# Performance work log

Measured on AMD Instinct MI355X. Metric: run time of the kernel, lower is better.

Reference implementation:

```python
import jax, jax.numpy as jnp
import numpy as np

N = 100_000   # nodes
E = 3_200_000 # edges (avg degree 32)
IN, HID, OUT = 1433, 16, 7  # hardcoded in Method_GCN_Class.__init__


def setup_inputs() -> dict:
    key = jax.random.key(0)
    ks = jax.random.split(key, 6)
    x = jax.random.normal(ks[0], (N, IN), dtype=jnp.float32)
    adj_row = jax.random.randint(ks[1], (E,), 0, N, dtype=jnp.int32)
    adj_col = jax.random.randint(ks[2], (E,), 0, N, dtype=jnp.int32)
    adj_val = jax.random.uniform(ks[3], (E,), dtype=jnp.float32)
    W1 = jax.random.uniform(ks[4], (IN, HID), dtype=jnp.float32)  # nn.init.uniform_
    b1 = jnp.zeros((HID,), dtype=jnp.float32)
    W2 = jax.random.uniform(ks[5], (HID, OUT), dtype=jnp.float32)
    b2 = jnp.zeros((OUT,), dtype=jnp.float32)
    return dict(x=x, adj_row=adj_row, adj_col=adj_col, adj_val=adj_val,
                W1=W1, b1=b1, W2=W2, b2=b2)


def _spmm(row, col, val, dense):
    # torch.sparse.mm(adj, dense) with adj in COO form: out[r] += val*dense[c]
    return jax.ops.segment_sum(val[:, None] * dense[col], row, num_segments=N)


def reference(x, adj_row, adj_col, adj_val, W1, b1, W2, b2):
    # layer 1: graph_conv -> relu (dropout p=0.1 is a no-op at inference)
    h = _spmm(adj_row, adj_col, adj_val, x @ W1) + b1
    h = jax.nn.relu(h)
    # layer 2: graph_conv -> log_softmax over classes
    h = _spmm(adj_row, adj_col, adj_val, h @ W2) + b2
    return jax.nn.log_softmax(h, axis=1)
```

## Files before the change

kernel.cpp:

```cpp
#include <hip/hip_runtime.h>
#include <math.h>

#define IN_F 1433
#define HID  16
#define OUTC 7
#define SCAN_T 1024

#define K1_THREADS 512
#define K1_ROWS_W  8
#define K1_ROWS_B  64
#define KA         768
#define LDSW       17
#define K1_LDS_FLOATS (KA * LDSW)

#define SLOT_C   44
#define OVF_CAP  131072

typedef float f4_t __attribute__((ext_vector_type(4)));
typedef f4_t uf4 __attribute__((aligned(4)));

__host__ __device__ __forceinline__ int imin(int a, int b) { return a < b ? a : b; }

__global__ __launch_bounds__(256) void zero_i32(int4* __restrict__ p, int n4)
{
    int i = blockIdx.x * blockDim.x + threadIdx.x;
    if (i < n4) p[i] = make_int4(0, 0, 0, 0);
}

__device__ __forceinline__ void k1_body(
    const float* __restrict__ x, const float* __restrict__ W1,
    float* __restrict__ XW, int N, int vbid, float* sW)
{
    const int wave = threadIdx.x >> 6;
    const int lane = threadIdx.x & 63;
    const int ks   = lane & 15;
    const int j4   = lane >> 4;
    const int row0 = vbid * K1_ROWS_B + wave * K1_ROWS_W;

    int xoff[K1_ROWS_W];
#pragma unroll
    for (int r = 0; r < K1_ROWS_W; ++r) {
        int row = row0 + r;
        if (row > N - 1) row = N - 1;
        if (row < 0) row = 0;
        xoff[r] = row * IN_F;
    }

    float acc[K1_ROWS_W][4];
#pragma unroll
    for (int r = 0; r < K1_ROWS_W; ++r)
#pragma unroll
        for (int jj = 0; jj < 4; ++jj) acc[r][jj] = 0.f;

#pragma unroll 1
    for (int p = 0; p < 2; ++p) {
        const int pbase = p ? KA : 0;
        const int pk    = p ? (IN_F - KA) : KA;
        if (p) __syncthreads();
        for (int f = threadIdx.x; f < pk * HID; f += K1_THREADS)
            sW[(f >> 4) * LDSW + (f & 15)] = W1[pbase * HID + f];
        __syncthreads();

        const int nfull = pk >> 6;
#pragma unroll 1
        for (int c = 0; c < nfull; ++c) {
            const int kb = c * 64 + ks * 4;
            uf4 xq[K1_ROWS_W];
#pragma unroll
            for (int r = 0; r < K1_ROWS_W; ++r)
                xq[r] = *(const uf4*)(x + (size_t)xoff[r] + pbase + kb);
            float w[4][4];
#pragma unroll
            for (int kk = 0; kk < 4; ++kk) {
                const float* wr = sW + (size_t)(kb + kk) * LDSW + j4 * 4;
                w[kk][0] = wr[0]; w[kk][1] = wr[1];
                w[kk][2] = wr[2]; w[kk][3] = wr[3];
            }
#pragma unroll
            for (int kk = 0; kk < 4; ++kk)
#pragma unroll
                for (int r = 0; r < K1_ROWS_W; ++r) {
                    const float xv = xq[r][kk];
                    acc[r][0] += xv * w[kk][0];
                    acc[r][1] += xv * w[kk][1];
                    acc[r][2] += xv * w[kk][2];
                    acc[r][3] += xv * w[kk][3];
                }
        }

        const int tb = nfull * 64 + ks * 4;
        if (tb < pk + 3 && (pk & 63)) {
#pragma unroll
            for (int kk = 0; kk < 4; ++kk) {
                const int kloc = tb + kk;
                const bool ok = (kloc < pk);
                const float* wr = sW + (size_t)kloc * LDSW + j4 * 4;
                float w0 = wr[0], w1 = wr[1], w2 = wr[2], w3 = wr[3];
#pragma unroll
                for (int r = 0; r < K1_ROWS_W; ++r) {
                    const float xv = ok ? x[(size_t)xoff[r] + pbase + kloc] : 0.f;
                    acc[r][0] += xv * w0;
                    acc[r][1] += xv * w1;
                    acc[r][2] += xv * w2;
                    acc[r][3] += xv * w3;
                }
            }
        }
    }

#pragma unroll
    for (int m = 1; m <= 8; m <<= 1)
#pragma unroll
        for (int r = 0; r < K1_ROWS_W; ++r)
#pragma unroll
            for (int jj = 0; jj < 4; ++jj)
                acc[r][jj] += __shfl_xor(acc[r][jj], m);

    if (ks == 0) {
#pragma unroll
        for (int r = 0; r < K1_ROWS_W; ++r) {
            const int row = row0 + r;
            if (row >= 0 && row < N) {
                float4 o = make_float4(acc[r][0], acc[r][1], acc[r][2], acc[r][3]);
                *(float4*)(XW + (size_t)row * HID + j4 * 4) = o;
            }
        }
    }
}

__device__ __forceinline__ void scatter_slots_body(
    const int* __restrict__ arow, const int* __restrict__ acol,
    const float* __restrict__ aval, int* __restrict__ cnt,
    int2* __restrict__ slots, int* __restrict__ ovf, int* __restrict__ ovfc,
    int E, int sb, int nsb)
{
    const int tid = sb * K1_THREADS + threadIdx.x;
    const int stride = nsb * K1_THREADS;
    const int E4 = E >> 2;
    const int4*   ar4 = (const int4*)arow;
    const int4*   ac4 = (const int4*)acol;
    const float4* av4 = (const float4*)aval;
    for (int v = tid; v < E4; v += stride) {
        int4 r = ar4[v];
        int4 c = ac4[v];
        float4 val = av4[v];
        int rr[4] = {r.x, r.y, r.z, r.w};
        int cc[4] = {c.x, c.y, c.z, c.w};
        float vv[4] = {val.x, val.y, val.z, val.w};
#pragma unroll
        for (int u = 0; u < 4; ++u) {
            int pos = atomicAdd(&cnt[rr[u]], 1);
            if (pos < SLOT_C) {
                slots[(size_t)rr[u] * SLOT_C + pos] =
                    make_int2(cc[u], __float_as_int(vv[u]));
            } else {
                int op = atomicAdd(ovfc, 1);
                if (op < OVF_CAP) {
                    ovf[3 * op]     = rr[u];
                    ovf[3 * op + 1] = cc[u];
                    ovf[3 * op + 2] = __float_as_int(vv[u]);
                }
            }
        }
    }
    for (int v = E4 * 4 + tid; v < E; v += stride) {
        int rr = arow[v];
        int pos = atomicAdd(&cnt[rr], 1);
        if (pos < SLOT_C) {
            slots[(size_t)rr * SLOT_C + pos] =
                make_int2(acol[v], __float_as_int(aval[v]));
        } else {
            int op = atomicAdd(ovfc, 1);
            if (op < OVF_CAP) {
                ovf[3 * op]     = rr;
                ovf[3 * op + 1] = acol[v];
                ovf[3 * op + 2] = __float_as_int(aval[v]);
            }
        }
    }
}

__global__ __launch_bounds__(K1_THREADS) void k1_scatter_slots(
    const float* __restrict__ x, const float* __restrict__ W1,
    float* __restrict__ XW, int N, int k1b,
    const int* __restrict__ arow, const int* __restrict__ acol,
    const float* __restrict__ aval, int* __restrict__ cnt,
    int2* __restrict__ slots, int* __restrict__ ovf, int* __restrict__ ovfc,
    int E, int scb)
{
    __shared__ float sW[K1_LDS_FLOATS];
    const int bid = blockIdx.x;
    if ((bid % 3 == 2) && (bid / 3 < scb)) {
        scatter_slots_body(arow, acol, aval, cnt, slots, ovf, ovfc, E, bid / 3, scb);
        return;
    }
    const int k1_idx = bid - imin((bid + 1) / 3, scb);
    if (k1_idx >= k1b) return;
    k1_body(x, W1, XW, N, k1_idx, sW);
}

__global__ __launch_bounds__(256) void ovf_apply16(
    const int* __restrict__ ovf, const int* __restrict__ ovfc,
    const float* __restrict__ XW, float* __restrict__ Hx)
{
    const int n = imin(ovfc[0], OVF_CAP);
    const int tid = blockIdx.x * blockDim.x + threadIdx.x;
    const int stride = gridDim.x * blockDim.x;
    for (int i = tid; i < n; i += stride) {
        const int r = ovf[3 * i], c = ovf[3 * i + 1];
        const float v = __int_as_float(ovf[3 * i + 2]);
        const float* src = XW + (size_t)c * HID;
        float* dst = Hx + (size_t)r * HID;
#pragma unroll
        for (int j = 0; j < HID; ++j) atomicAdd(dst + j, v * src[j]);
    }
}

__global__ __launch_bounds__(256) void ovf_apply7(
    const int* __restrict__ ovf, const int* __restrict__ ovfc,
    const float* __restrict__ h2, float* __restrict__ Ox)
{
    const int n = imin(ovfc[0], OVF_CAP);
    const int tid = blockIdx.x * blockDim.x + threadIdx.x;
    const int stride = gridDim.x * blockDim.x;
    for (int i = tid; i < n; i += stride) {
        const int r = ovf[3 * i], c = ovf[3 * i + 1];
        const float v = __int_as_float(ovf[3 * i + 2]);
        const float* src = h2 + (size_t)c * 8;
        float* dst = Ox + (size_t)r * 8;
#pragma unroll
        for (int j = 0; j < OUTC; ++j) atomicAdd(dst + j, v * src[j]);
    }
}

__global__ __launch_bounds__(256) void spmm16_slots(
    const int* __restrict__ cnt, const int2* __restrict__ slots,
    const float* __restrict__ XW, const float* __restrict__ Hx,
    const float* __restrict__ b1, const float* __restrict__ W2,
    float* __restrict__ h2, int N)
{
    const int gw = (int)((blockIdx.x * (size_t)blockDim.x + threadIdx.x) >> 6);
    if (gw >= N) return;
    const int lane = threadIdx.x & 63;
    const int j = lane & 15;
    const int w = lane >> 4;
    int deg = cnt[gw]; deg = deg < SLOT_C ? deg : SLOT_C;
    const int2* base = slots + (size_t)gw * SLOT_C;

    float acc = 0.f;
    int k = w * 4;
    while (k + 4 <= deg) {
        const int4* q = (const int4*)(base + k);
        int4 A = q[0], B = q[1];
        acc += __int_as_float(A.y) * XW[(size_t)A.x * HID + j];
        acc += __int_as_float(A.w) * XW[(size_t)A.z * HID + j];
        acc += __int_as_float(B.y) * XW[(size_t)B.x * HID + j];
        acc += __int_as_float(B.w) * XW[(size_t)B.z * HID + j];
        k += 16;
    }
    for (; k < deg; ++k) {
        int2 a = base[k];
        acc += __int_as_float(a.y) * XW[(size_t)a.x * HID + j];
    }
    acc += __shfl_xor(acc, 16);
    acc += __shfl_xor(acc, 32);
    acc += Hx[(size_t)gw * HID + j];

    const float h = fmaxf(acc + b1[j], 0.f);
    float p[OUTC];
#pragma unroll
    for (int c = 0; c < OUTC; ++c) p[c] = h * W2[j * OUTC + c];
#pragma unroll
    for (int m = 1; m <= 8; m <<= 1)
#pragma unroll
        for (int c = 0; c < OUTC; ++c) p[c] += __shfl_xor(p[c], m);

    if (lane < 8) {
        float o = p[0];
        o = (lane == 1) ? p[1] : o;
        o = (lane == 2) ? p[2] : o;
        o = (lane == 3) ? p[3] : o;
        o = (lane == 4) ? p[4] : o;
        o = (lane == 5) ? p[5] : o;
        o = (lane == 6) ? p[6] : o;
        if (lane == 7) o = 0.f;
        h2[(size_t)gw * 8 + lane] = o;
    }
}

__global__ __launch_bounds__(256) void spmm7_slots(
    const int* __restrict__ cnt, const int2* __restrict__ slots,
    const float* __restrict__ h2, const float* __restrict__ Ox,
    const float* __restrict__ b2, float* __restrict__ out, int N)
{
    const int gw = (int)((blockIdx.x * (size_t)blockDim.x + threadIdx.x) >> 6);
    if (gw >= N) return;
    const int lane = threadIdx.x & 63;
    const int j = lane & 7;
    const int w = lane >> 3;
    int deg = cnt[gw]; deg = deg < SLOT_C ? deg : SLOT_C;
    const int2* base = slots + (size_t)gw * SLOT_C;

    float acc = 0.f;
    int k = w * 4;
    while (k + 4 <= deg) {
        const int4* q = (const int4*)(base + k);
        int4 A = q[0], B = q[1];
        acc += __int_as_float(A.y) * h2[(size_t)A.x * 8 + j];
        acc += __int_as_float(A.w) * h2[(size_t)A.z * 8 + j];
        acc += __int_as_float(B.y) * h2[(size_t)B.x * 8 + j];
        acc += __int_as_float(B.w) * h2[(size_t)B.z * 8 + j];
        k += 32;
    }
    for (; k < deg; ++k) {
        int2 a = base[k];
        acc += __int_as_float(a.y) * h2[(size_t)a.x * 8 + j];
    }
    acc += __shfl_xor(acc, 8);
    acc += __shfl_xor(acc, 16);
    acc += __shfl_xor(acc, 32);
    acc += Ox[(size_t)gw * 8 + j];

    const float bias = b2[(j < OUTC) ? j : 0];
    const float val  = acc + bias;
    float mx = (j < OUTC) ? val : -INFINITY;
    mx = fmaxf(mx, __shfl_xor(mx, 1));
    mx = fmaxf(mx, __shfl_xor(mx, 2));
    mx = fmaxf(mx, __shfl_xor(mx, 4));
    float ex = (j < OUTC) ? expf(val - mx) : 0.f;
    ex += __shfl_xor(ex, 1);
    ex += __shfl_xor(ex, 2);
    ex += __shfl_xor(ex, 4);
    if (lane < OUTC) out[(size_t)gw * OUTC + lane] = val - mx - logf(ex);
}

__device__ __forceinline__ void hist_body(
    const int* __restrict__ arow, int* __restrict__ cnt, int E, int hb, int nhb)
{
    const int tid = hb * K1_THREADS + threadIdx.x;
    const int stride = nhb * K1_THREADS;
    const int E4 = E >> 2;
    const int4* a4 = (const int4*)arow;
    for (int v = tid; v < E4; v += stride) {
        int4 r = a4[v];
        atomicAdd(&cnt[r.x], 1);
        atomicAdd(&cnt[r.y], 1);
        atomicAdd(&cnt[r.z], 1);
        atomicAdd(&cnt[r.w], 1);
    }
    for (int v = E4 * 4 + tid; v < E; v += stride) atomicAdd(&cnt[arow[v]], 1);
}

__device__ __forceinline__ void scatter_body(
    const int* __restrict__ arow, const int* __restrict__ acol,
    const float* __restrict__ aval, int* __restrict__ cursor,
    int2* __restrict__ ecv, int E, int sb, int nsb)
{
    const int tid = sb * K1_THREADS + threadIdx.x;
    const int stride = nsb * K1_THREADS;
    const int E4 = E >> 2;
    const int4*   ar4 = (const int4*)arow;
    const int4*   ac4 = (const int4*)acol;
    const float4* av4 = (const float4*)aval;
    for (int v = tid; v < E4; v += stride) {
        int4 r = ar4[v];
        int4 c = ac4[v];
        float4 val = av4[v];
        int p0 = atomicAdd(&cursor[r.x], 1);
        int p1 = atomicAdd(&cursor[r.y], 1);
        int p2 = atomicAdd(&cursor[r.z], 1);
        int p3 = atomicAdd(&cursor[r.w], 1);
        ecv[p0] = make_int2(c.x, __float_as_int(val.x));
        ecv[p1] = make_int2(c.y, __float_as_int(val.y));
        ecv[p2] = make_int2(c.z, __float_as_int(val.z));
        ecv[p3] = make_int2(c.w, __float_as_int(val.w));
    }
    for (int v = E4 * 4 + tid; v < E; v += stride) {
        int pos = atomicAdd(&cursor[arow[v]], 1);
        ecv[pos] = make_int2(acol[v], __float_as_int(aval[v]));
    }
}

__global__ __launch_bounds__(K1_THREADS) void k1_hist_fused(
    const float* __restrict__ x, const float* __restrict__ W1,
    float* __restrict__ XW, int N, int half1,
    const int* __restrict__ arow, int* __restrict__ cnt, int E, int histB)
{
    __shared__ float sW[K1_LDS_FLOATS];
    const int bid = blockIdx.x;
    if ((bid % 3 == 2) && (bid / 3 < histB)) {
        hist_body(arow, cnt, E, bid / 3, histB);
        return;
    }
    const int k1_idx = bid - imin((bid + 1) / 3, histB);
    if (k1_idx >= half1) return;
    k1_body(x, W1, XW, N, k1_idx, sW);
}

__global__ __launch_bounds__(K1_THREADS) void k1_scatter_fused(
    const float* __restrict__ x, const float* __restrict__ W1,
    float* __restrict__ XW, int N, int half1, int half2,
    const int* __restrict__ arow, const int* __restrict__ acol,
    const float* __restrict__ aval, int* __restrict__ cursor,
    int2* __restrict__ ecv, int E, int scb)
{
    __shared__ float sW[K1_LDS_FLOATS];
    const int bid = blockIdx.x;
    if ((bid % 3 == 2) && (bid / 3 < scb)) {
        scatter_body(arow, acol, aval, cursor, ecv, E, bid / 3, scb);
        return;
    }
    const int k1_idx = bid - imin((bid + 1) / 3, scb) + half1;
    if (k1_idx >= half1 + half2) return;
    k1_body(x, W1, XW, N, k1_idx, sW);
}

__global__ __launch_bounds__(K1_THREADS) void gcn_k1_xw(
    const float* __restrict__ x, const float* __restrict__ W1,
    float* __restrict__ XW, int N)
{
    __shared__ float sW[K1_LDS_FLOATS];
    k1_body(x, W1, XW, N, blockIdx.x, sW);
}

__global__ __launch_bounds__(256) void csr_hist(
    const int* __restrict__ arow, int* __restrict__ cnt, int E)
{
    int e = blockIdx.x * blockDim.x + threadIdx.x;
    if (e < E) atomicAdd(&cnt[arow[e]], 1);
}

__global__ __launch_bounds__(256) void csr_scatter(
    const int* __restrict__ arow, const int* __restrict__ acol,
    const float* __restrict__ aval, int* __restrict__ cursor,
    int2* __restrict__ ecv, int E)
{
    int e = blockIdx.x * blockDim.x + threadIdx.x;
    if (e >= E) return;
    int pos = atomicAdd(&cursor[arow[e]], 1);
    ecv[pos] = make_int2(acol[e], __float_as_int(aval[e]));
}

__global__ __launch_bounds__(SCAN_T) void csr_scan(
    const int* __restrict__ cnt, int* __restrict__ rowptr,
    int* __restrict__ cursor, int N)
{
    __shared__ int sums[SCAN_T];
    const int t = threadIdx.x;
    const int chunk = (((N + SCAN_T - 1) / SCAN_T) + 3) & ~3;
    const int lo = t * chunk;
    int s = 0;
    const bool full = (lo + chunk <= N);
    if (full) {
        const int4* c4 = (const int4*)(cnt + lo);
#pragma unroll 4
        for (int i = 0; i < chunk / 4; ++i) {
            int4 v = c4[i];
            s += ((v.x + 1) & ~1) + ((v.y + 1) & ~1)
               + ((v.z + 1) & ~1) + ((v.w + 1) & ~1);
        }
    } else {
        const int hi = (lo + chunk < N) ? lo + chunk : N;
        for (int i = lo; i < hi; ++i) s += (cnt[i] + 1) & ~1;
    }
    sums[t] = s;
    __syncthreads();
    for (int d = 1; d < SCAN_T; d <<= 1) {
        int a = sums[t];
        int b = (t >= d) ? sums[t - d] : 0;
        __syncthreads();
        sums[t] = a + b;
        __syncthreads();
    }
    int run = sums[t] - s;
    if (full) {
        const int4* c4 = (const int4*)(cnt + lo);
        int4* rp4 = (int4*)(rowptr + lo);
        int4* cu4 = (int4*)(cursor + lo);
        for (int i = 0; i < chunk / 4; ++i) {
            int4 v = c4[i];
            int4 o;
            o.x = run; run += (v.x + 1) & ~1;
            o.y = run; run += (v.y + 1) & ~1;
            o.z = run; run += (v.z + 1) & ~1;
            o.w = run; run += (v.w + 1) & ~1;
            rp4[i] = o;
            cu4[i] = o;
        }
    } else {
        const int hi = (lo + chunk < N) ? lo + chunk : N;
        for (int i = lo; i < hi; ++i) {
            rowptr[i] = run;
            cursor[i] = run;
            run += (cnt[i] + 1) & ~1;
        }
    }
    if (t == SCAN_T - 1) rowptr[N] = sums[SCAN_T - 1];
}

__global__ __launch_bounds__(256) void spmm16_h2(
    const int* __restrict__ rowptr, const int2* __restrict__ ecv,
    const float* __restrict__ XW, const float* __restrict__ b1,
    const float* __restrict__ W2, float* __restrict__ h2, int N)
{
    const int gw = (int)((blockIdx.x * (size_t)blockDim.x + threadIdx.x) >> 6);
    if (gw >= N) return;
    const int lane = threadIdx.x & 63;
    const int j = lane & 15;
    const int w = lane >> 4;
    const int s = rowptr[gw], e = rowptr[gw + 1];

    float acc = 0.f;
    int k = s + w * 4;
    while (k + 4 <= e) {
        const int4* q = (const int4*)(ecv + k);
        int4 A = q[0], B = q[1];
        acc += __int_as_float(A.y) * XW[(size_t)A.x * HID + j];
        acc += __int_as_float(A.w) * XW[(size_t)A.z * HID + j];
        acc += __int_as_float(B.y) * XW[(size_t)B.x * HID + j];
        acc += __int_as_float(B.w) * XW[(size_t)B.z * HID + j];
        k += 16;
    }
    for (; k < e; ++k) {
        int2 a = ecv[k];
        acc += __int_as_float(a.y) * XW[(size_t)a.x * HID + j];
    }
    acc += __shfl_xor(acc, 16);
    acc += __shfl_xor(acc, 32);

    const float h = fmaxf(acc + b1[j], 0.f);
    float p[OUTC];
#pragma unroll
    for (int c = 0; c < OUTC; ++c) p[c] = h * W2[j * OUTC + c];
#pragma unroll
    for (int m = 1; m <= 8; m <<= 1)
#pragma unroll
        for (int c = 0; c < OUTC; ++c) p[c] += __shfl_xor(p[c], m);

    if (lane < 8) {
        float o = p[0];
        o = (lane == 1) ? p[1] : o;
        o = (lane == 2) ? p[2] : o;
        o = (lane == 3) ? p[3] : o;
        o = (lane == 4) ? p[4] : o;
        o = (lane == 5) ? p[5] : o;
        o = (lane == 6) ? p[6] : o;
        if (lane == 7) o = 0.f;
        h2[(size_t)gw * 8 + lane] = o;
    }
}

__global__ __launch_bounds__(256) void spmm7_lsm(
    const int* __restrict__ rowptr, const int2* __restrict__ ecv,
    const float* __restrict__ h2, const float* __restrict__ b2,
    float* __restrict__ out, int N)
{
    const int gw = (int)((blockIdx.x * (size_t)blockDim.x + threadIdx.x) >> 6);
    if (gw >= N) return;
    const int lane = threadIdx.x & 63;
    const int j = lane & 7;
    const int w = lane >> 3;
    const int s = rowptr[gw], e = rowptr[gw + 1];

    float acc = 0.f;
    int k = s + w * 4;
    while (k + 4 <= e) {
        const int4* q = (const int4*)(ecv + k);
        int4 A = q[0], B = q[1];
        acc += __int_as_float(A.y) * h2[(size_t)A.x * 8 + j];
        acc += __int_as_float(A.w) * h2[(size_t)A.z * 8 + j];
        acc += __int_as_float(B.y) * h2[(size_t)B.x * 8 + j];
        acc += __int_as_float(B.w) * h2[(size_t)B.z * 8 + j];
        k += 32;
    }
    for (; k < e; ++k) {
        int2 a = ecv[k];
        acc += __int_as_float(a.y) * h2[(size_t)a.x * 8 + j];
    }
    acc += __shfl_xor(acc, 8);
    acc += __shfl_xor(acc, 16);
    acc += __shfl_xor(acc, 32);

    const float bias = b2[(j < OUTC) ? j : 0];
    const float val  = acc + bias;
    float mx = (j < OUTC) ? val : -INFINITY;
    mx = fmaxf(mx, __shfl_xor(mx, 1));
    mx = fmaxf(mx, __shfl_xor(mx, 2));
    mx = fmaxf(mx, __shfl_xor(mx, 4));
    float ex = (j < OUTC) ? expf(val - mx) : 0.f;
    ex += __shfl_xor(ex, 1);
    ex += __shfl_xor(ex, 2);
    ex += __shfl_xor(ex, 4);
    if (lane < OUTC) out[(size_t)gw * OUTC + lane] = val - mx - logf(ex);
}

__global__ __launch_bounds__(256) void gcn_k2_spmm16_atomic(
    const int* __restrict__ arow, const int* __restrict__ acol,
    const float* __restrict__ aval, const float* __restrict__ XW,
    float* __restrict__ H, int E)
{
    int e = blockIdx.x * blockDim.x + threadIdx.x;
    if (e >= E) return;
    const int r = arow[e], c = acol[e];
    const float v = aval[e];
    const float4* src = (const float4*)(XW + (size_t)c * HID);
    float4 a = src[0], b = src[1], cc = src[2], d = src[3];
    float* dst = H + (size_t)r * HID;
    atomicAdd(dst + 0,  v * a.x);  atomicAdd(dst + 1,  v * a.y);
    atomicAdd(dst + 2,  v * a.z);  atomicAdd(dst + 3,  v * a.w);
    atomicAdd(dst + 4,  v * b.x);  atomicAdd(dst + 5,  v * b.y);
    atomicAdd(dst + 6,  v * b.z);  atomicAdd(dst + 7,  v * b.w);
    atomicAdd(dst + 8,  v * cc.x); atomicAdd(dst + 9,  v * cc.y);
    atomicAdd(dst + 10, v * cc.z); atomicAdd(dst + 11, v * cc.w);
    atomicAdd(dst + 12, v * d.x);  atomicAdd(dst + 13, v * d.y);
    atomicAdd(dst + 14, v * d.z);  atomicAdd(dst + 15, v * d.w);
}

__global__ __launch_bounds__(256) void gcn_k3_h2(
    const float* __restrict__ H, const float* __restrict__ b1,
    const float* __restrict__ W2, float* __restrict__ h2, int N)
{
    __shared__ float sW2[HID * OUTC];
    __shared__ float sb1[HID];
    if (threadIdx.x < HID * OUTC) sW2[threadIdx.x] = W2[threadIdx.x];
    if (threadIdx.x < HID)        sb1[threadIdx.x] = b1[threadIdx.x];
    __syncthreads();

    int row = blockIdx.x * blockDim.x + threadIdx.x;
    if (row >= N) return;

    const float4* hp = (const float4*)(H + (size_t)row * HID);
    float4 h0 = hp[0], h1 = hp[1], h2v = hp[2], h3 = hp[3];
    float h[16] = {h0.x, h0.y, h0.z, h0.w, h1.x, h1.y, h1.z, h1.w,
                   h2v.x, h2v.y, h2v.z, h2v.w, h3.x, h3.y, h3.z, h3.w};
#pragma unroll
    for (int i = 0; i < HID; ++i) {
        h[i] += sb1[i];
        h[i] = h[i] > 0.f ? h[i] : 0.f;
    }
    float o[8];
#pragma unroll
    for (int jj = 0; jj < OUTC; ++jj) {
        float sum = 0.f;
#pragma unroll
        for (int i = 0; i < HID; ++i) sum += h[i] * sW2[i * OUTC + jj];
        o[jj] = sum;
    }
    o[7] = 0.f;
    float4* op = (float4*)(h2 + (size_t)row * 8);
    op[0] = make_float4(o[0], o[1], o[2], o[3]);
    op[1] = make_float4(o[4], o[5], o[6], o[7]);
}

__global__ __launch_bounds__(256) void gcn_k4_spmm7_atomic(
    const int* __restrict__ arow, const int* __restrict__ acol,
    const float* __restrict__ aval, const float* __restrict__ h2,
    float* __restrict__ out, int E)
{
    int e = blockIdx.x * blockDim.x + threadIdx.x;
    if (e >= E) return;
    const int r = arow[e], c = acol[e];
    const float v = aval[e];
    const float* src = h2 + (size_t)c * 8;
    float* dst = out + (size_t)r * OUTC;
#pragma unroll
    for (int jj = 0; jj < OUTC; ++jj) atomicAdd(dst + jj, v * src[jj]);
}

__global__ __launch_bounds__(256) void gcn_k5_lsm(
    float* __restrict__ out, const float* __restrict__ b2, int N)
{
    int row = blockIdx.x * blockDim.x + threadIdx.x;
    if (row >= N) return;
    float* p = out + (size_t)row * OUTC;
    float v[OUTC];
#pragma unroll
    for (int jj = 0; jj < OUTC; ++jj) v[jj] = p[jj] + b2[jj];
    float m = v[0];
#pragma unroll
    for (int jj = 1; jj < OUTC; ++jj) m = fmaxf(m, v[jj]);
    float s = 0.f;
#pragma unroll
    for (int jj = 0; jj < OUTC; ++jj) s += expf(v[jj] - m);
    const float ls = logf(s);
#pragma unroll
    for (int jj = 0; jj < OUTC; ++jj) p[jj] = v[jj] - m - ls;
}

extern "C" void kernel_launch(void* const* d_in, const int* in_sizes, int n_in,
                              void* d_out, int out_size, void* d_ws, size_t ws_size,
                              hipStream_t stream)
{
    const float* x    = (const float*)d_in[0];
    const int*   arow = (const int*)d_in[1];
    const int*   acol = (const int*)d_in[2];
    const float* aval = (const float*)d_in[3];
    const float* W1   = (const float*)d_in[4];
    const float* b1   = (const float*)d_in[5];
    const float* W2   = (const float*)d_in[6];
    const float* b2   = (const float*)d_in[7];
    float* out = (float*)d_out;

    const int N = in_sizes[0] / IN_F;
    const int E = in_sizes[1];

    const int Np4 = (N + 3) & ~3;
    const int eb  = (E + 255) / 256;
    const int nb  = (N + 255) / 256;
    const int k1b = (N + K1_ROWS_B - 1) / K1_ROWS_B;
    const int scb1 = imin(512, k1b / 3);

    {
        char* wsp = (char*)d_ws;
        int2*  slots = (int2*)wsp;  wsp += (size_t)N * SLOT_C * 8;
        float* XW    = (float*)wsp; wsp += (size_t)N * HID * 4;
        float* h2    = (float*)wsp; wsp += (size_t)N * 8 * 4;
        int*   ovf   = (int*)wsp;   wsp += (size_t)OVF_CAP * 12;
        char*  zbase = wsp;
        int*   cnt   = (int*)wsp;   wsp += (size_t)Np4 * 4;
        float* Hx    = (float*)wsp; wsp += (size_t)N * HID * 4;
        float* Ox    = (float*)wsp; wsp += (size_t)N * 8 * 4;
        int*   ovfc  = (int*)wsp;   wsp += 16;
        const size_t need1 = (size_t)(wsp - (char*)d_ws);

        if (ws_size >= need1 && scb1 >= 1) {
            const size_t zbytes = (size_t)(wsp - zbase);
            const int n4z = (int)(zbytes / 16);
            zero_i32<<<(n4z + 255) / 256, 256, 0, stream>>>((int4*)zbase, n4z);

            k1_scatter_slots<<<k1b + scb1, K1_THREADS, 0, stream>>>(
                x, W1, XW, N, k1b, arow, acol, aval, cnt, slots, ovf, ovfc, E, scb1);
            ovf_apply16<<<128, 256, 0, stream>>>(ovf, ovfc, XW, Hx);
            spmm16_slots<<<(N + 3) / 4, 256, 0, stream>>>(
                cnt, slots, XW, Hx, b1, W2, h2, N);
            ovf_apply7<<<128, 256, 0, stream>>>(ovf, ovfc, h2, Ox);
            spmm7_slots<<<(N + 3) / 4, 256, 0, stream>>>(
                cnt, slots, h2, Ox, b2, out, N);
            return;
        }
    }

    {
        const int EPAD = E + N + 8;
        char* wsp = (char*)d_ws;
        int2*  ecv    = (int2*)wsp;   wsp += (size_t)EPAD * 8;
        int*   cnt    = (int*)wsp;    wsp += (size_t)Np4 * 4;
        int*   cursor = (int*)wsp;    wsp += (size_t)Np4 * 4;
        int*   rowptr = (int*)wsp;    wsp += (size_t)(Np4 + 4) * 4;
        float* XW     = (float*)wsp;  wsp += (size_t)N * HID * 4;
        float* h2     = (float*)wsp;  wsp += (size_t)N * 8 * 4;
        const size_t need2 = (size_t)(wsp - (char*)d_ws);

        if (ws_size >= need2) {
            const size_t zbytes = (size_t)EPAD * 8 + (size_t)Np4 * 4;
            const int n4z = (int)((zbytes + 15) / 16);
            zero_i32<<<(n4z + 255) / 256, 256, 0, stream>>>((int4*)d_ws, n4z);

            const int half1 = (k1b + 1) / 2;
            const int half2 = k1b - half1;
            const int histB = imin(384, half1 / 2);
            const int scb   = imin(384, half2 / 2);

            if (histB >= 1 && scb >= 1) {
                k1_hist_fused<<<half1 + histB, K1_THREADS, 0, stream>>>(
                    x, W1, XW, N, half1, arow, cnt, E, histB);
                csr_scan<<<1, SCAN_T, 0, stream>>>(cnt, rowptr, cursor, N);
                k1_scatter_fused<<<half2 + scb, K1_THREADS, 0, stream>>>(
                    x, W1, XW, N, half1, half2, arow, acol, aval, cursor, ecv, E, scb);
            } else {
                csr_hist<<<eb, 256, 0, stream>>>(arow, cnt, E);
                csr_scan<<<1, SCAN_T, 0, stream>>>(cnt, rowptr, cursor, N);
                csr_scatter<<<eb, 256, 0, stream>>>(arow, acol, aval, cursor, ecv, E);
                gcn_k1_xw<<<k1b, K1_THREADS, 0, stream>>>(x, W1, XW, N);
            }

            spmm16_h2<<<(N + 3) / 4, 256, 0, stream>>>(rowptr, ecv, XW, b1, W2, h2, N);
            spmm7_lsm<<<(N + 3) / 4, 256, 0, stream>>>(rowptr, ecv, h2, b2, out, N);
            return;
        }
    }

    {
        float* XWf = (float*)d_ws;
        float* Hf  = XWf + (size_t)N * HID;
        float* h2f = XWf;
        const int hz4 = (int)(((size_t)N * HID) / 4);
        zero_i32<<<(hz4 + 255) / 256, 256, 0, stream>>>((int4*)Hf, hz4);
        (void)hipMemsetAsync(out, 0, (size_t)N * OUTC * sizeof(float), stream);
        gcn_k1_xw<<<k1b, K1_THREADS, 0, stream>>>(x, W1, XWf, N);
        gcn_k2_spmm16_atomic<<<eb, 256, 0, stream>>>(arow, acol, aval, XWf, Hf, E);
        gcn_k3_h2<<<nb, 256, 0, stream>>>(Hf, b1, W2, h2f, N);
        gcn_k4_spmm7_atomic<<<eb, 256, 0, stream>>>(arow, acol, aval, h2f, out, E);
        gcn_k5_lsm<<<nb, 256, 0, stream>>>(out, b2, N);
    }
}
```

Before: 430.9 us.

## Replace per-row edge slots with 128-row bucket partition and LDS-atomic SpMM

Instead of scattering each edge into a fixed per-row slot array with one global atomic per edge, edges are partitioned in chunks into 128-row buckets. Each chunk builds an LDS histogram and then makes one global atomic per bucket, and the packed row-local index and column share one int. The SpMM kernels now run one block per bucket and accumulate into shared memory with LDS atomics, then do the bias, ReLU and W2 product or the log-softmax per row. This cuts global atomic contention and the scattered slot writes. The cost is heavy LDS atomic traffic, an extra fallback condition (N up to 2^17), and a changed split between the partition and GEMM blocks.

```diff
diff --git a/kernel.cpp b/kernel.cpp
--- a/kernel.cpp
+++ b/kernel.cpp
@@ -13,7 +13,9 @@
 #define LDSW       17
 #define K1_LDS_FLOATS (KA * LDSW)
 
-#define SLOT_C   44
+#define RPB      128
+#define BCAP     4480
+#define PCH      2048
 #define OVF_CAP  131072
 
 typedef float f4_t __attribute__((ext_vector_type(4)));
@@ -128,31 +130,52 @@
     }
 }
 
-__device__ __forceinline__ void scatter_slots_body(
+__device__ __forceinline__ void partition_body(
     const int* __restrict__ arow, const int* __restrict__ acol,
-    const float* __restrict__ aval, int* __restrict__ cnt,
-    int2* __restrict__ slots, int* __restrict__ ovf, int* __restrict__ ovfc,
-    int E, int sb, int nsb)
-{
-    const int tid = sb * K1_THREADS + threadIdx.x;
-    const int stride = nsb * K1_THREADS;
-    const int E4 = E >> 2;
-    const int4*   ar4 = (const int4*)arow;
-    const int4*   ac4 = (const int4*)acol;
-    const float4* av4 = (const float4*)aval;
-    for (int v = tid; v < E4; v += stride) {
-        int4 r = ar4[v];
-        int4 c = ac4[v];
-        float4 val = av4[v];
-        int rr[4] = {r.x, r.y, r.z, r.w};
-        int cc[4] = {c.x, c.y, c.z, c.w};
-        float vv[4] = {val.x, val.y, val.z, val.w};
-#pragma unroll
-        for (int u = 0; u < 4; ++u) {
-            int pos = atomicAdd(&cnt[rr[u]], 1);
-            if (pos < SLOT_C) {
-                slots[(size_t)rr[u] * SLOT_C + pos] =
-                    make_int2(cc[u], __float_as_int(vv[u]));
+    const float* __restrict__ aval, int* __restrict__ cursor,
+    int2* __restrict__ buckets, int* __restrict__ ovf, int* __restrict__ ovfc,
+    int E, int nbuk, int sb, int nsb, int* hist)
+{
+    const int nch = (E + PCH - 1) / PCH;
+    for (int ch = sb; ch < nch; ch += nsb) {
+        const int e0 = ch * PCH;
+        const int e1 = imin(e0 + PCH, E);
+        for (int b = threadIdx.x; b < nbuk; b += K1_THREADS) hist[b] = 0;
+        __syncthreads();
+
+        int rr[4], cc[4]; float vv[4];
+        int nl = 0;
+        const int base = e0 + threadIdx.x * 4;
+        if (base + 3 < e1) {
+            int4 r4 = *(const int4*)(arow + base);
+            int4 c4 = *(const int4*)(acol + base);
+            float4 v4 = *(const float4*)(aval + base);
+            rr[0]=r4.x; rr[1]=r4.y; rr[2]=r4.z; rr[3]=r4.w;
+            cc[0]=c4.x; cc[1]=c4.y; cc[2]=c4.z; cc[3]=c4.w;
+            vv[0]=v4.x; vv[1]=v4.y; vv[2]=v4.z; vv[3]=v4.w;
+            nl = 4;
+        } else {
+            for (int i = base; i < e1 && nl < 4; ++i) {
+                rr[nl] = arow[i]; cc[nl] = acol[i]; vv[nl] = aval[i];
+                ++nl;
+            }
+        }
+        for (int u = 0; u < nl; ++u) atomicAdd(&hist[rr[u] >> 7], 1);
+        __syncthreads();
+
+        for (int b = threadIdx.x; b < nbuk; b += K1_THREADS) {
+            const int h = hist[b];
+            hist[b] = (h > 0) ? atomicAdd(&cursor[b], h) : 0;
+        }
+        __syncthreads();
+
+        for (int u = 0; u < nl; ++u) {
+            const int b = rr[u] >> 7;
+            const int pos = atomicAdd(&hist[b], 1);
+            if (pos < BCAP) {
+                buckets[(size_t)b * BCAP + pos] =
+                    make_int2(((rr[u] & (RPB - 1)) << 17) | cc[u],
+                              __float_as_int(vv[u]));
             } else {
                 int op = atomicAdd(ovfc, 1);
                 if (op < OVF_CAP) {
@@ -162,39 +185,26 @@
                 }
             }
         }
-    }
-    for (int v = E4 * 4 + tid; v < E; v += stride) {
-        int rr = arow[v];
-        int pos = atomicAdd(&cnt[rr], 1);
-        if (pos < SLOT_C) {
-            slots[(size_t)rr * SLOT_C + pos] =
-                make_int2(acol[v], __float_as_int(aval[v]));
-        } else {
-            int op = atomicAdd(ovfc, 1);
-            if (op < OVF_CAP) {
-                ovf[3 * op]     = rr;
-                ovf[3 * op + 1] = acol[v];
-                ovf[3 * op + 2] = __float_as_int(aval[v]);
-            }
-        }
-    }
-}
-
-__global__ __launch_bounds__(K1_THREADS) void k1_scatter_slots(
+        __syncthreads();
+    }
+}
+
+__global__ __launch_bounds__(K1_THREADS) void k1_partition(
     const float* __restrict__ x, const float* __restrict__ W1,
     float* __restrict__ XW, int N, int k1b,
     const int* __restrict__ arow, const int* __restrict__ acol,
-    const float* __restrict__ aval, int* __restrict__ cnt,
-    int2* __restrict__ slots, int* __restrict__ ovf, int* __restrict__ ovfc,
-    int E, int scb)
+    const float* __restrict__ aval, int* __restrict__ cursor,
+    int2* __restrict__ buckets, int* __restrict__ ovf, int* __restrict__ ovfc,
+    int E, int nbuk, int scb)
 {
     __shared__ float sW[K1_LDS_FLOATS];
     const int bid = blockIdx.x;
-    if ((bid % 3 == 2) && (bid / 3 < scb)) {
-        scatter_slots_body(arow, acol, aval, cnt, slots, ovf, ovfc, E, bid / 3, scb);
+    if ((bid % 4 == 3) && (bid / 4 < scb)) {
+        partition_body(arow, acol, aval, cursor, buckets, ovf, ovfc,
+                       E, nbuk, bid / 4, scb, (int*)sW);
         return;
     }
-    const int k1_idx = bid - imin((bid + 1) / 3, scb);
+    const int k1_idx = bid - imin((bid + 1) / 4, scb);
     if (k1_idx >= k1b) return;
     k1_body(x, W1, XW, N, k1_idx, sW);
 }
@@ -233,105 +243,117 @@
     }
 }
 
-__global__ __launch_bounds__(256) void spmm16_slots(
-    const int* __restrict__ cnt, const int2* __restrict__ slots,
+__global__ __launch_bounds__(512) void spmmB16(
+    const int* __restrict__ cursor, const int2* __restrict__ buckets,
     const float* __restrict__ XW, const float* __restrict__ Hx,
     const float* __restrict__ b1, const float* __restrict__ W2,
     float* __restrict__ h2, int N)
 {
-    const int gw = (int)((blockIdx.x * (size_t)blockDim.x + threadIdx.x) >> 6);
-    if (gw >= N) return;
-    const int lane = threadIdx.x & 63;
-    const int j = lane & 15;
-    const int w = lane >> 4;
-    int deg = cnt[gw]; deg = deg < SLOT_C ? deg : SLOT_C;
-    const int2* base = slots + (size_t)gw * SLOT_C;
-
-    float acc = 0.f;
-    int k = w * 4;
-    while (k + 4 <= deg) {
-        const int4* q = (const int4*)(base + k);
-        int4 A = q[0], B = q[1];
-        acc += __int_as_float(A.y) * XW[(size_t)A.x * HID + j];
-        acc += __int_as_float(A.w) * XW[(size_t)A.z * HID + j];
-        acc += __int_as_float(B.y) * XW[(size_t)B.x * HID + j];
-        acc += __int_as_float(B.w) * XW[(size_t)B.z * HID + j];
-        k += 16;
-    }
-    for (; k < deg; ++k) {
-        int2 a = base[k];
-        acc += __int_as_float(a.y) * XW[(size_t)a.x * HID + j];
-    }
-    acc += __shfl_xor(acc, 16);
-    acc += __shfl_xor(acc, 32);
-    acc += Hx[(size_t)gw * HID + j];
-
-    const float h = fmaxf(acc + b1[j], 0.f);
-    float p[OUTC];
-#pragma unroll
-    for (int c = 0; c < OUTC; ++c) p[c] = h * W2[j * OUTC + c];
-#pragma unroll
-    for (int m = 1; m <= 8; m <<= 1)
-#pragma unroll
-        for (int c = 0; c < OUTC; ++c) p[c] += __shfl_xor(p[c], m);
-
-    if (lane < 8) {
-        float o = p[0];
-        o = (lane == 1) ? p[1] : o;
-        o = (lane == 2) ? p[2] : o;
-        o = (lane == 3) ? p[3] : o;
-        o = (lane == 4) ? p[4] : o;
-        o = (lane == 5) ? p[5] : o;
-        o = (lane == 6) ? p[6] : o;
-        if (lane == 7) o = 0.f;
-        h2[(size_t)gw * 8 + lane] = o;
-    }
-}
-
-__global__ __launch_bounds__(256) void spmm7_slots(
-    const int* __restrict__ cnt, const int2* __restrict__ slots,
+    __shared__ float acc[RPB * 17];
+    __shared__ float sW2[HID * OUTC];
+    __shared__ float sb1[HID];
+    const int b = blockIdx.x;
+    if (threadIdx.x < HID * OUTC) sW2[threadIdx.x] = W2[threadIdx.x];
+    if (threadIdx.x < HID)        sb1[threadIdx.x] = b1[threadIdx.x];
+    for (int i = threadIdx.x; i < RPB * 17; i += 512) acc[i] = 0.f;
+    __syncthreads();
+
+    const int cnt_b = imin(cursor[b], BCAP);
+    const int2* base = buckets + (size_t)b * BCAP;
+    for (int i = threadIdx.x; i < cnt_b; i += 512) {
+        const int2 ed = base[i];
+        const int c  = ed.x & 0x1FFFF;
+        const int rl = ed.x >> 17;
+        const float v = __int_as_float(ed.y);
+        const float4* xp = (const float4*)(XW + (size_t)c * HID);
+        float4 a = xp[0], q = xp[1], s = xp[2], d = xp[3];
+        float* ar = acc + rl * 17;
+        atomicAdd(ar + 0,  v * a.x);  atomicAdd(ar + 1,  v * a.y);
+        atomicAdd(ar + 2,  v * a.z);  atomicAdd(ar + 3,  v * a.w);
+        atomicAdd(ar + 4,  v * q.x);  atomicAdd(ar + 5,  v * q.y);
+        atomicAdd(ar + 6,  v * q.z);  atomicAdd(ar + 7,  v * q.w);
+        atomicAdd(ar + 8,  v * s.x);  atomicAdd(ar + 9,  v * s.y);
+        atomicAdd(ar + 10, v * s.z);  atomicAdd(ar + 11, v * s.w);
+        atomicAdd(ar + 12, v * d.x);  atomicAdd(ar + 13, v * d.y);
+        atomicAdd(ar + 14, v * d.z);  atomicAdd(ar + 15, v * d.w);
+    }
+    __syncthreads();
+
+    const int t = threadIdx.x;
+    if (t < RPB) {
+        const int row = b * RPB + t;
+        if (row < N) {
+            float h[16];
+#pragma unroll
+            for (int j = 0; j < HID; ++j) {
+                const float s2 = acc[t * 17 + j] + Hx[(size_t)row * HID + j] + sb1[j];
+                h[j] = s2 > 0.f ? s2 : 0.f;
+            }
+            float o[8];
+#pragma unroll
+            for (int jj = 0; jj < OUTC; ++jj) {
+                float s2 = 0.f;
+#pragma unroll
+                for (int i2 = 0; i2 < HID; ++i2) s2 += h[i2] * sW2[i2 * OUTC + jj];
+                o[jj] = s2;
+            }
+            o[7] = 0.f;
+            float4* op = (float4*)(h2 + (size_t)row * 8);
+            op[0] = make_float4(o[0], o[1], o[2], o[3]);
+            op[1] = make_float4(o[4], o[5], o[6], o[7]);
+        }
+    }
+}
+
+__global__ __launch_bounds__(512) void spmmB7(
+    const int* __restrict__ cursor, const int2* __restrict__ buckets,
     const float* __restrict__ h2, const float* __restrict__ Ox,
     const float* __restrict__ b2, float* __restrict__ out, int N)
 {
-    const int gw = (int)((blockIdx.x * (size_t)blockDim.x + threadIdx.x) >> 6);
-    if (gw >= N) return;
-    const int lane = threadIdx.x & 63;
-    const int j = lane & 7;
-    const int w = lane >> 3;
-    int deg = cnt[gw]; deg = deg < SLOT_C ? deg : SLOT_C;
-    const int2* base = slots + (size_t)gw * SLOT_C;
-
-    float acc = 0.f;
-    int k = w * 4;
-    while (k + 4 <= deg) {
-        const int4* q = (const int4*)(base + k);
-        int4 A = q[0], B = q[1];
-        acc += __int_as_float(A.y) * h2[(size_t)A.x * 8 + j];
-        acc += __int_as_float(A.w) * h2[(size_t)A.z * 8 + j];
-        acc += __int_as_float(B.y) * h2[(size_t)B.x * 8 + j];
-        acc += __int_as_float(B.w) * h2[(size_t)B.z * 8 + j];
-        k += 32;
-    }
-    for (; k < deg; ++k) {
-        int2 a = base[k];
-        acc += __int_as_float(a.y) * h2[(size_t)a.x * 8 + j];
-    }
-    acc += __shfl_xor(acc, 8);
-    acc += __shfl_xor(acc, 16);
-    acc += __shfl_xor(acc, 32);
-    acc += Ox[(size_t)gw * 8 + j];
-
-    const float bias = b2[(j < OUTC) ? j : 0];
-    const float val  = acc + bias;
-    float mx = (j < OUTC) ? val : -INFINITY;
-    mx = fmaxf(mx, __shfl_xor(mx, 1));
-    mx = fmaxf(mx, __shfl_xor(mx, 2));
-    mx = fmaxf(mx, __shfl_xor(mx, 4));
-    float ex = (j < OUTC) ? expf(val - mx) : 0.f;
-    ex += __shfl_xor(ex, 1);
-    ex += __shfl_xor(ex, 2);
-    ex += __shfl_xor(ex, 4);
-    if (lane < OUTC) out[(size_t)gw * OUTC + lane] = val - mx - logf(ex);
+    __shared__ float acc[RPB * 9];
+    __shared__ float sb2[8];
+    const int b = blockIdx.x;
+    if (threadIdx.x < OUTC) sb2[threadIdx.x] = b2[threadIdx.x];
+    for (int i = threadIdx.x; i < RPB * 9; i += 512) acc[i] = 0.f;
+    __syncthreads();
+
+    const int cnt_b = imin(cursor[b], BCAP);
+    const int2* base = buckets + (size_t)b * BCAP;
+    for (int i = threadIdx.x; i < cnt_b; i += 512) {
+        const int2 ed = base[i];
+        const int c  = ed.x & 0x1FFFF;
+        const int rl = ed.x >> 17;
+        const float v = __int_as_float(ed.y);
+        const float4* hp = (const float4*)(h2 + (size_t)c * 8);
+        float4 a = hp[0], q = hp[1];
+        float* ar = acc + rl * 9;
+        atomicAdd(ar + 0, v * a.x); atomicAdd(ar + 1, v * a.y);
+        atomicAdd(ar + 2, v * a.z); atomicAdd(ar + 3, v * a.w);
+        atomicAdd(ar + 4, v * q.x); atomicAdd(ar + 5, v * q.y);
+        atomicAdd(ar + 6, v * q.z);
+    }
+    __syncthreads();
+
+    const int t = threadIdx.x;
+    if (t < RPB) {
+        const int row = b * RPB + t;
+        if (row < N) {
+            float vj[OUTC];
+#pragma unroll
+            for (int j = 0; j < OUTC; ++j)
+                vj[j] = acc[t * 9 + j] + Ox[(size_t)row * 8 + j] + sb2[j];
+            float m = vj[0];
+#pragma unroll
+            for (int j = 1; j < OUTC; ++j) m = fmaxf(m, vj[j]);
+            float s = 0.f;
+#pragma unroll
+            for (int j = 0; j < OUTC; ++j) s += expf(vj[j] - m);
+            const float ls = logf(s);
+            float* p = out + (size_t)row * OUTC;
+#pragma unroll
+            for (int j = 0; j < OUTC; ++j) p[j] = vj[j] - m - ls;
+        }
+    }
 }
 
 __device__ __forceinline__ void hist_body(
@@ -708,34 +730,35 @@
     const int eb  = (E + 255) / 256;
     const int nb  = (N + 255) / 256;
     const int k1b = (N + K1_ROWS_B - 1) / K1_ROWS_B;
-    const int scb1 = imin(512, k1b / 3);
+    const int nbuk = (N + RPB - 1) / RPB;
+    const int scb1 = imin(384, k1b / 4);
 
     {
         char* wsp = (char*)d_ws;
-        int2*  slots = (int2*)wsp;  wsp += (size_t)N * SLOT_C * 8;
-        float* XW    = (float*)wsp; wsp += (size_t)N * HID * 4;
-        float* h2    = (float*)wsp; wsp += (size_t)N * 8 * 4;
-        int*   ovf   = (int*)wsp;   wsp += (size_t)OVF_CAP * 12;
-        char*  zbase = wsp;
-        int*   cnt   = (int*)wsp;   wsp += (size_t)Np4 * 4;
-        float* Hx    = (float*)wsp; wsp += (size_t)N * HID * 4;
-        float* Ox    = (float*)wsp; wsp += (size_t)N * 8 * 4;
-        int*   ovfc  = (int*)wsp;   wsp += 16;
+        int2*  buckets = (int2*)wsp;  wsp += (size_t)nbuk * BCAP * 8;
+        float* XW      = (float*)wsp; wsp += (size_t)N * HID * 4;
+        float* h2      = (float*)wsp; wsp += (size_t)N * 8 * 4;
+        int*   ovf     = (int*)wsp;   wsp += (size_t)OVF_CAP * 12;
+        char*  zbase   = wsp;
+        int*   cursor  = (int*)wsp;   wsp += (size_t)((nbuk + 3) & ~3) * 4;
+        float* Hx      = (float*)wsp; wsp += (size_t)N * HID * 4;
+        float* Ox      = (float*)wsp; wsp += (size_t)N * 8 * 4;
+        int*   ovfc    = (int*)wsp;   wsp += 16;
         const size_t need1 = (size_t)(wsp - (char*)d_ws);
 
-        if (ws_size >= need1 && scb1 >= 1) {
+        if (ws_size >= need1 && scb1 >= 1 && N <= (1 << 17) &&
+            nbuk <= K1_LDS_FLOATS) {
             const size_t zbytes = (size_t)(wsp - zbase);
             const int n4z = (int)(zbytes / 16);
             zero_i32<<<(n4z + 255) / 256, 256, 0, stream>>>((int4*)zbase, n4z);
 
-            k1_scatter_slots<<<k1b + scb1, K1_THREADS, 0, stream>>>(
-                x, W1, XW, N, k1b, arow, acol, aval, cnt, slots, ovf, ovfc, E, scb1);
+            k1_partition<<<k1b + scb1, K1_THREADS, 0, stream>>>(
+                x, W1, XW, N, k1b, arow, acol, aval, cursor, buckets,
+                ovf, ovfc, E, nbuk, scb1);
             ovf_apply16<<<128, 256, 0, stream>>>(ovf, ovfc, XW, Hx);
-            spmm16_slots<<<(N + 3) / 4, 256, 0, stream>>>(
-                cnt, slots, XW, Hx, b1, W2, h2, N);
+            spmmB16<<<nbuk, 512, 0, stream>>>(cursor, buckets, XW, Hx, b1, W2, h2, N);
             ovf_apply7<<<128, 256, 0, stream>>>(ovf, ovfc, h2, Ox);
-            spmm7_slots<<<(N + 3) / 4, 256, 0, stream>>>(
-                cnt, slots, h2, Ox, b2, out, N);
+            spmmB7<<<nbuk, 512, 0, stream>>>(cursor, buckets, h2, Ox, b2, out, N);
             return;
         }
     }
```

New measurement: 745.9 us. 73.1% more time.
